# Kernel optimization log

Measured on AMD Instinct MI355X. Metric: run time of the kernel, lower is better.

The kernel has to match this reference:

```python
import jax, jax.numpy as jnp
import numpy as np

N = 100000      # nodes
E = 1600000     # edges (avg degree 16)
F_IN = 64
HID = 128
OUT = 64


def setup_inputs() -> dict:
    key = jax.random.key(0)
    ks = jax.random.split(key, 12)
    s = lambda k, i, o: jax.random.normal(k, (i, o), jnp.float32) / np.sqrt(i)
    x = jax.random.normal(ks[0], (N, F_IN), jnp.float32)
    edge_index = jax.random.randint(ks[1], (2, E), 0, N, dtype=jnp.int64)
    return {
        "x": x,
        "edge_index": edge_index,
        # conv1: SAGEConv(F_IN -> HID): lin_l (neighbors, with bias), lin_r (root)
        "W1n": s(ks[2], F_IN, HID), "b1n": jnp.zeros((HID,), jnp.float32),
        "W1r": s(ks[3], F_IN, HID),
        # lin1: Linear(F_IN -> HID)
        "Wl1": s(ks[4], F_IN, HID), "bl1": jnp.zeros((HID,), jnp.float32),
        # conv2: SAGEConv(HID -> OUT)
        "W2n": s(ks[5], HID, OUT), "b2n": jnp.zeros((OUT,), jnp.float32),
        "W2r": s(ks[6], HID, OUT),
        # lin2: Linear(HID -> OUT)
        "Wl2": s(ks[7], HID, OUT), "bl2": jnp.zeros((OUT,), jnp.float32),
    }


def _sage(x, src, dst, Wn, bn, Wr):
    # mean aggregation of source-node features at destination nodes
    msg = x[src]                                             # [E, F]
    agg = jax.ops.segment_sum(msg, dst, num_segments=N)      # [N, F]
    deg = jax.ops.segment_sum(jnp.ones((src.shape[0],), x.dtype), dst,
                              num_segments=N)                # [N]
    mean = agg / jnp.maximum(deg, 1.0)[:, None]
    return mean @ Wn + bn + x @ Wr


def reference(x, edge_index, W1n, b1n, W1r, Wl1, bl1, W2n, b2n, W2r, Wl2, bl2):
    src, dst = edge_index[0], edge_index[1]
    h = _sage(x, src, dst, W1n, b1n, W1r) + (x @ Wl1 + bl1)
    h = jax.nn.relu(h)
    out = _sage(h, src, dst, W2n, b2n, W2r) + (h @ Wl2 + bl2)
    return out
```

## Files before the change

### kernel.cpp

```cpp
#include <hip/hip_runtime.h>


#define NN 100000
#define NE 1600000
#define NSB 98
#define CAP2 18432
#define EPB 6250
#define MB 256
#define WPB 128

typedef __attribute__((ext_vector_type(8))) __bf16 bf16x8;
typedef __attribute__((ext_vector_type(4))) float f32x4;

__device__ __forceinline__ float b2f(unsigned short u) {
    unsigned v = ((unsigned)u) << 16;
    float f;
    __builtin_memcpy(&f, &v, 4);
    return f;
}
__device__ __forceinline__ float b2f_lo(unsigned v) {
    unsigned w = v << 16;
    float f;
    __builtin_memcpy(&f, &w, 4);
    return f;
}
__device__ __forceinline__ float b2f_hi(unsigned v) {
    unsigned w = v & 0xFFFF0000u;
    float f;
    __builtin_memcpy(&f, &w, 4);
    return f;
}
__device__ __forceinline__ unsigned short f2b(float f) {
    unsigned u;
    __builtin_memcpy(&u, &f, 4);
    u += 0x7FFFu + ((u >> 16) & 1u);
    return (unsigned short)(u >> 16);
}

__global__ void sniff_kernel(const int* __restrict__ ei,
                             const unsigned int* __restrict__ xw,
                             int* __restrict__ flags, int* __restrict__ cntP) {
    __shared__ int s_or[256];
    __shared__ int s_cnt[256];
    int tid = threadIdx.x;
    if (tid < NSB) cntP[tid * 16] = 0;
    s_or[tid] = ei[2 * tid + 1];
    unsigned e = (xw[tid] >> 7) & 0xFFu;
    s_cnt[tid] = (e > 0x85u) ? 1 : 0;
    __syncthreads();
    for (int s = 128; s > 0; s >>= 1) {
        if (tid < s) { s_or[tid] |= s_or[tid + s]; s_cnt[tid] += s_cnt[tid + s]; }
        __syncthreads();
    }
    if (tid == 0) {
        flags[0] = (s_or[0] == 0) ? 1 : 0;
        flags[1] = (s_cnt[0] >= 32) ? 1 : 0;
    }
}

__global__ __launch_bounds__(256) void prep_kernel(
    const void* __restrict__ x, const int* __restrict__ flags,
    const void* W1n, const void* W1r, const void* Wl1,
    const void* b1n, const void* bl1,
    const void* W2n, const void* W2r, const void* Wl2,
    const void* b2n, const void* bl2,
    unsigned short* __restrict__ Wt1g, unsigned short* __restrict__ Wt2g,
    float* __restrict__ bias1, float* __restrict__ bias2,
    unsigned int* __restrict__ xbu) {
    bool fp32 = flags[1] != 0;
    int tid = threadIdx.x;
    if (blockIdx.x >= WPB) {
        int t = (blockIdx.x - WPB) * 256 + tid;
        if (t >= NN * 8) return;
        if (fp32) {
            const float4* xf = (const float4*)x;
            float4 a = xf[2 * t], b = xf[2 * t + 1];
            uint4 o;
            o.x = f2b(a.x) | ((unsigned)f2b(a.y) << 16);
            o.y = f2b(a.z) | ((unsigned)f2b(a.w) << 16);
            o.z = f2b(b.x) | ((unsigned)f2b(b.y) << 16);
            o.w = f2b(b.z) | ((unsigned)f2b(b.w) << 16);
            ((uint4*)xbu)[t] = o;
        } else {
            ((uint4*)xbu)[t] = ((const uint4*)x)[t];
        }
        return;
    }
    auto rd = [&](const void* p, int i) -> float {
        return fp32 ? ((const float*)p)[i] : b2f(((const unsigned short*)p)[i]);
    };
    if (blockIdx.x < 64) {
        int idx = blockIdx.x * 256 + tid;
        int c = idx >> 7, k = idx & 127;
        float v = (k < 64) ? rd(W1n, k * 128 + c)
                           : rd(W1r, (k - 64) * 128 + c) + rd(Wl1, (k - 64) * 128 + c);
        Wt1g[c * 128 + k] = f2b(v);
        if (blockIdx.x == 0 && tid < 128) bias1[tid] = rd(b1n, tid) + rd(bl1, tid);
    } else {
        int idx = (blockIdx.x - 64) * 256 + tid;
        int c = idx >> 7, k = idx & 127;
        float v = (c < 64) ? rd(W2n, k * 64 + c)
                           : rd(W2r, k * 64 + (c - 64)) + rd(Wl2, k * 64 + (c - 64));
        Wt2g[c * 128 + k] = f2b(v);
        if (blockIdx.x == 64 && tid < 64) bias2[tid] = rd(b2n, tid) + rd(bl2, tid);
    }
}


__global__ __launch_bounds__(512) void bscatter_kernel(
    const int* __restrict__ ei, const int* __restrict__ flags,
    int* __restrict__ cntP, int* __restrict__ ebuf) {
    __shared__ int lh[NSB];
    __shared__ int lbase[NSB];
    int t = threadIdx.x;
    if (t < NSB) lh[t] = 0;
    __syncthreads();
    int e0 = blockIdx.x * EPB;
    bool i64 = flags[0] != 0;
    for (int i = t; i < EPB; i += 512) {
        int e = e0 + i;
        int d = i64 ? (int)((const long long*)ei)[NE + e] : ei[NE + e];
        atomicAdd(&lh[d >> 10], 1);
    }
    __syncthreads();
    if (t < NSB) {
        int c = lh[t];
        lbase[t] = c ? atomicAdd(&cntP[t * 16], c) : 0;
        lh[t] = 0;
    }
    __syncthreads();
    for (int i = t; i < EPB; i += 512) {
        int e = e0 + i;
        int s, d;
        if (i64) { const long long* q = (const long long*)ei; s = (int)q[e]; d = (int)q[NE + e]; }
        else     { s = ei[e]; d = ei[NE + e]; }
        int sb = d >> 10;
        int r = lbase[sb] + atomicAdd(&lh[sb], 1);
        if (r < CAP2) ebuf[sb * CAP2 + r] = (s << 10) | (d & 1023);
    }
}

__global__ __launch_bounds__(512) void csr_build_kernel(
    const int* __restrict__ ebuf, const int* __restrict__ cntP,
    int* __restrict__ rpack, int* __restrict__ csr) {
    __shared__ int lcnt[1024];
    __shared__ int lsum[512];
    __shared__ int lcur[1024];
    int t = threadIdx.x, b = blockIdx.x;
    lcnt[t] = 0; lcnt[t + 512] = 0;
    __syncthreads();
    int base = b * CAP2;
    int cnt = min(cntP[b * 16], CAP2);
    for (int i = t; i < cnt; i += 512) atomicAdd(&lcnt[ebuf[base + i] & 1023], 1);
    __syncthreads();
    int c0 = lcnt[2 * t], c1 = lcnt[2 * t + 1];
    lsum[t] = c0 + c1;
    __syncthreads();
    for (int off = 1; off < 512; off <<= 1) {
        int v = lsum[t];
        int add = (t >= off) ? lsum[t - off] : 0;
        __syncthreads();
        lsum[t] = v + add;
        __syncthreads();
    }
    int excl = (t == 0) ? 0 : lsum[t - 1];
    int ex0 = excl, ex1 = excl + c0;
    lcur[2 * t] = ex0; lcur[2 * t + 1] = ex1;
    int d0 = b * 1024 + 2 * t;
    if (d0 < NN)     rpack[d0]     = ((base + ex0) << 8) | min(c0, 255);
    if (d0 + 1 < NN) rpack[d0 + 1] = ((base + ex1) << 8) | min(c1, 255);
    __syncthreads();
    for (int i = t; i < cnt; i += 512) {
        int pk = ebuf[base + i];
        int r = atomicAdd(&lcur[pk & 1023], 1);
        csr[base + r] = pk >> 10;
    }
}


__device__ __forceinline__ void gather_acc(
    const unsigned short* __restrict__ feat, const int* __restrict__ csr,
    int base, int deg, int fo, float* acc) {
    int t = 0;
    for (; t + 8 <= deg; t += 8) {
        int i0 = csr[base + t],     i1 = csr[base + t + 1];
        int i2 = csr[base + t + 2], i3 = csr[base + t + 3];
        int i4 = csr[base + t + 4], i5 = csr[base + t + 5];
        int i6 = csr[base + t + 6], i7 = csr[base + t + 7];
        bf16x8 v0 = *(const bf16x8*)(feat + (size_t)i0 * 64 + fo);
        bf16x8 v1 = *(const bf16x8*)(feat + (size_t)i1 * 64 + fo);
        bf16x8 v2 = *(const bf16x8*)(feat + (size_t)i2 * 64 + fo);
        bf16x8 v3 = *(const bf16x8*)(feat + (size_t)i3 * 64 + fo);
        bf16x8 v4 = *(const bf16x8*)(feat + (size_t)i4 * 64 + fo);
        bf16x8 v5 = *(const bf16x8*)(feat + (size_t)i5 * 64 + fo);
        bf16x8 v6 = *(const bf16x8*)(feat + (size_t)i6 * 64 + fo);
        bf16x8 v7 = *(const bf16x8*)(feat + (size_t)i7 * 64 + fo);
#pragma unroll
        for (int k = 0; k < 8; ++k)
            acc[k] += (((float)v0[k] + (float)v1[k]) + ((float)v2[k] + (float)v3[k]))
                    + (((float)v4[k] + (float)v5[k]) + ((float)v6[k] + (float)v7[k]));
    }
    for (; t + 4 <= deg; t += 4) {
        int i0 = csr[base + t],     i1 = csr[base + t + 1];
        int i2 = csr[base + t + 2], i3 = csr[base + t + 3];
        bf16x8 v0 = *(const bf16x8*)(feat + (size_t)i0 * 64 + fo);
        bf16x8 v1 = *(const bf16x8*)(feat + (size_t)i1 * 64 + fo);
        bf16x8 v2 = *(const bf16x8*)(feat + (size_t)i2 * 64 + fo);
        bf16x8 v3 = *(const bf16x8*)(feat + (size_t)i3 * 64 + fo);
#pragma unroll
        for (int k = 0; k < 8; ++k)
            acc[k] += ((float)v0[k] + (float)v1[k]) + ((float)v2[k] + (float)v3[k]);
    }
    for (; t < deg; ++t) {
        int i = csr[base + t];
        bf16x8 v = *(const bf16x8*)(feat + (size_t)i * 64 + fo);
#pragma unroll
        for (int k = 0; k < 8; ++k) acc[k] += (float)v[k];
    }
}

__global__ __launch_bounds__(256) void agg1_kernel(
    const unsigned short* __restrict__ feat, const int* __restrict__ rpack,
    const int* __restrict__ csr, unsigned int* __restrict__ mean1u) {
    int wid = threadIdx.x >> 6, lane = threadIdx.x & 63;
    int slot = lane >> 3, fo = (lane & 7) * 8;
    int d = (blockIdx.x * 4 + wid) * 8 + slot;
    int dd = min(d, NN - 1);
    int rp = rpack[dd];
    int base = rp >> 8;
    int deg = rp & 255;
    float acc[8];
#pragma unroll
    for (int k = 0; k < 8; ++k) acc[k] = 0.f;
    gather_acc(feat, csr, base, deg, fo, acc);
    if (d < NN) {
        float r = 1.0f / fmaxf((float)deg, 1.0f);
        uint4 o;
        o.x = f2b(acc[0] * r) | ((unsigned)f2b(acc[1] * r) << 16);
        o.y = f2b(acc[2] * r) | ((unsigned)f2b(acc[3] * r) << 16);
        o.z = f2b(acc[4] * r) | ((unsigned)f2b(acc[5] * r) << 16);
        o.w = f2b(acc[6] * r) | ((unsigned)f2b(acc[7] * r) << 16);
        *(uint4*)(mean1u + (size_t)d * 32 + (lane & 7) * 4) = o;
    }
}

__global__ __launch_bounds__(256) void agg2_kernel(
    const unsigned short* __restrict__ p, const int* __restrict__ rpack,
    const int* __restrict__ csr, const unsigned int* __restrict__ sfu,
    const float* __restrict__ bias2, const int* __restrict__ flags,
    void* __restrict__ out) {
    int wid = threadIdx.x >> 6, lane = threadIdx.x & 63;
    int slot = lane >> 3, fo = (lane & 7) * 8;
    int d = (blockIdx.x * 4 + wid) * 8 + slot;
    int dd = min(d, NN - 1);
    int rp = rpack[dd];
    int base = rp >> 8;
    int deg = rp & 255;
    float acc[8];
#pragma unroll
    for (int k = 0; k < 8; ++k) acc[k] = 0.f;
    gather_acc(p, csr, base, deg, fo, acc);
    if (d < NN) {
        float r = 1.0f / fmaxf((float)deg, 1.0f);
        uint4 sv = *(const uint4*)(sfu + (size_t)d * 32 + (lane & 7) * 4);
        float4 bA = *(const float4*)(bias2 + fo);
        float4 bB = *(const float4*)(bias2 + fo + 4);
        float v0 = acc[0] * r + b2f_lo(sv.x) + bA.x;
        float v1 = acc[1] * r + b2f_hi(sv.x) + bA.y;
        float v2 = acc[2] * r + b2f_lo(sv.y) + bA.z;
        float v3 = acc[3] * r + b2f_hi(sv.y) + bA.w;
        float v4 = acc[4] * r + b2f_lo(sv.z) + bB.x;
        float v5 = acc[5] * r + b2f_hi(sv.z) + bB.y;
        float v6 = acc[6] * r + b2f_lo(sv.w) + bB.z;
        float v7 = acc[7] * r + b2f_hi(sv.w) + bB.w;
        if (flags[1]) {
            float* op = (float*)out + (size_t)d * 64 + fo;
            *(float4*)op = make_float4(v0, v1, v2, v3);
            *(float4*)(op + 4) = make_float4(v4, v5, v6, v7);
        } else {
            uint4 o;
            o.x = f2b(v0) | ((unsigned)f2b(v1) << 16);
            o.y = f2b(v2) | ((unsigned)f2b(v3) << 16);
            o.z = f2b(v4) | ((unsigned)f2b(v5) << 16);
            o.w = f2b(v6) | ((unsigned)f2b(v7) << 16);
            *(uint4*)((unsigned int*)out + (size_t)d * 32 + (lane & 7) * 4) = o;
        }
    }
}

__global__ __launch_bounds__(512, 2) void gemmF_kernel(
    const unsigned short* __restrict__ mean1,
    const unsigned short* __restrict__ xb,
    const unsigned short* __restrict__ Wt1g, const float* __restrict__ bias1,
    const unsigned short* __restrict__ Wt2g,
    unsigned short* __restrict__ p, unsigned short* __restrict__ sf) {
    __shared__ unsigned short Wt1s[128 * 136];
    __shared__ unsigned short Wt2s[128 * 136];
    __shared__ unsigned short hs[MB * 136];
    int tid = threadIdx.x;
    int wid = tid >> 6, lane = tid & 63;
    int m = lane & 15, g = lane >> 4;
    int row0 = blockIdx.x * MB + wid * 32;

    bf16x8 a_frag[2][4];
#pragma unroll
    for (int t = 0; t < 2; ++t) {
        int arow = min(row0 + t * 16 + m, NN - 1);
#pragma unroll
        for (int kt = 0; kt < 4; ++kt) {
            int k0 = kt * 32 + g * 8;
            a_frag[t][kt] = (k0 < 64)
                ? *(const bf16x8*)(mean1 + (size_t)arow * 64 + k0)
                : *(const bf16x8*)(xb + (size_t)arow * 64 + (k0 - 64));
        }
    }

    for (int idx = tid; idx < 4096; idx += 512) {
        int c = (idx >> 4) & 127, ch = idx & 15;
        if (idx < 2048)
            *(bf16x8*)&Wt1s[c * 136 + ch * 8] = *(const bf16x8*)&Wt1g[c * 128 + ch * 8];
        else
            *(bf16x8*)&Wt2s[c * 136 + ch * 8] = *(const bf16x8*)&Wt2g[c * 128 + ch * 8];
    }
    __syncthreads();

    f32x4 acc[2][8];
#pragma unroll
    for (int t = 0; t < 2; ++t)
#pragma unroll
        for (int nt = 0; nt < 8; ++nt) acc[t][nt] = (f32x4){0.f, 0.f, 0.f, 0.f};

#pragma unroll
    for (int kt = 0; kt < 4; ++kt) {
        int k0 = kt * 32 + g * 8;
        bf16x8 b[8];
#pragma unroll
        for (int nt = 0; nt < 8; ++nt)
            b[nt] = *(const bf16x8*)(&Wt1s[(nt * 16 + m) * 136 + k0]);
#pragma unroll
        for (int nt = 0; nt < 8; ++nt) {
            acc[0][nt] = __builtin_amdgcn_mfma_f32_16x16x32_bf16(a_frag[0][kt], b[nt], acc[0][nt], 0, 0, 0);
            acc[1][nt] = __builtin_amdgcn_mfma_f32_16x16x32_bf16(a_frag[1][kt], b[nt], acc[1][nt], 0, 0, 0);
        }
    }

#pragma unroll
    for (int t = 0; t < 2; ++t)
#pragma unroll
        for (int nt = 0; nt < 8; ++nt) {
            int col = nt * 16 + m;
            float bias = bias1[col];
#pragma unroll
            for (int r = 0; r < 4; ++r) {
                float v = fmaxf(acc[t][nt][r] + bias, 0.0f);
                hs[(wid * 32 + t * 16 + g * 4 + r) * 136 + col] = f2b(v);
            }
        }

    bf16x8 a2[2][4];
#pragma unroll
    for (int t = 0; t < 2; ++t)
#pragma unroll
        for (int kt = 0; kt < 4; ++kt)
            a2[t][kt] = *(const bf16x8*)(&hs[(wid * 32 + t * 16 + m) * 136 + kt * 32 + g * 8]);

#pragma unroll
    for (int t = 0; t < 2; ++t)
#pragma unroll
        for (int nt = 0; nt < 8; ++nt) acc[t][nt] = (f32x4){0.f, 0.f, 0.f, 0.f};

#pragma unroll
    for (int kt = 0; kt < 4; ++kt) {
        int k0 = kt * 32 + g * 8;
        bf16x8 b[8];
#pragma unroll
        for (int nt = 0; nt < 8; ++nt)
            b[nt] = *(const bf16x8*)(&Wt2s[(nt * 16 + m) * 136 + k0]);
#pragma unroll
        for (int nt = 0; nt < 8; ++nt) {
            acc[0][nt] = __builtin_amdgcn_mfma_f32_16x16x32_bf16(a2[0][kt], b[nt], acc[0][nt], 0, 0, 0);
            acc[1][nt] = __builtin_amdgcn_mfma_f32_16x16x32_bf16(a2[1][kt], b[nt], acc[1][nt], 0, 0, 0);
        }
    }

#pragma unroll
    for (int t = 0; t < 2; ++t)
#pragma unroll
        for (int nt = 0; nt < 8; ++nt) {
            int col = nt * 16 + m;
#pragma unroll
            for (int r = 0; r < 4; ++r) {
                int row2 = row0 + t * 16 + g * 4 + r;
                if (row2 < NN) {
                    float v = acc[t][nt][r];
                    if (col < 64) p[(size_t)row2 * 64 + col] = f2b(v);
                    else          sf[(size_t)row2 * 64 + (col - 64)] = f2b(v);
                }
            }
        }
}

extern "C" void kernel_launch(void* const* d_in, const int* in_sizes, int n_in,
                              void* d_out, int out_size, void* d_ws, size_t ws_size,
                              hipStream_t stream) {
    const void* x   = d_in[0];
    const int*  ei  = (const int*)d_in[1];
    const void* W1n = d_in[2];
    const void* b1n = d_in[3];
    const void* W1r = d_in[4];
    const void* Wl1 = d_in[5];
    const void* bl1 = d_in[6];
    const void* W2n = d_in[7];
    const void* b2n = d_in[8];
    const void* W2r = d_in[9];
    const void* Wl2 = d_in[10];
    const void* bl2 = d_in[11];

    char* ws = (char*)d_ws;
    int*            flags = (int*)(ws + 0);
    int*            cntP  = (int*)(ws + 1024);
    int*            rpack = (int*)(ws + 8192);
    float*          bias1 = (float*)(ws + 409600);
    float*          bias2 = (float*)(ws + 410112);
    unsigned short* Wt1g  = (unsigned short*)(ws + 410368);
    unsigned short* Wt2g  = (unsigned short*)(ws + 443136);
    int*            csr   = (int*)(ws + 475904);
    unsigned short* xb    = (unsigned short*)(ws + 7701248);
    unsigned short* p     = xb;
    unsigned short* mean1 = (unsigned short*)(ws + 20501248);
    unsigned short* sf    = (unsigned short*)(ws + 33301248);
    int*            ebuf  = (int*)(ws + 46101248);

    (void)in_sizes; (void)n_in; (void)out_size; (void)ws_size;

    sniff_kernel<<<1, 256, 0, stream>>>(ei, (const unsigned int*)x, flags, cntP);
    prep_kernel<<<WPB + (NN * 8 + 255) / 256, 256, 0, stream>>>(
        x, flags, W1n, W1r, Wl1, b1n, bl1, W2n, W2r, Wl2, b2n, bl2,
        Wt1g, Wt2g, bias1, bias2, (unsigned int*)xb);
    bscatter_kernel<<<256, 512, 0, stream>>>(ei, flags, cntP, ebuf);
    csr_build_kernel<<<NSB, 512, 0, stream>>>(ebuf, cntP, rpack, csr);
    agg1_kernel<<<(NN + 31) / 32, 256, 0, stream>>>(xb, rpack, csr, (unsigned int*)mean1);
    gemmF_kernel<<<(NN + MB - 1) / MB, 512, 0, stream>>>(mean1, xb, Wt1g, bias1, Wt2g, p, sf);
    agg2_kernel<<<(NN + 31) / 32, 256, 0, stream>>>(p, rpack, csr, (const unsigned int*)sf,
                                                    bias2, flags, d_out);
}
```

Baseline: 232.2 us.

## Fuse sniff, prep and edge bucketing into one front kernel

Merges the dtype-sniff, weight/input conversion and edge bucket-scatter kernels into one launch with role-partitioned blocks. Each block recomputes the int64 or fp32 detection locally, and the counter reset moves to a memset. Scatter blocks cache destination indices in shared memory so the second pass does not re-read them from global memory. The extra LDS per block may lower occupancy for the scatter role, and every block repeats the small sniff reduction.

```diff
diff --git a/kernel.cpp b/kernel.cpp
--- a/kernel.cpp
+++ b/kernel.cpp
@@ -7,7 +7,10 @@
 #define CAP2 18432
 #define EPB 6250
 #define MB 256
-#define WPB 128
+#define BSB 256
+#define W1B 32
+#define W2B 32
+#define XBLK ((NN * 8 + 511) / 512)
 
 typedef __attribute__((ext_vector_type(8))) __bf16 bf16x8;
 typedef __attribute__((ext_vector_type(4))) float f32x4;
@@ -37,106 +40,106 @@
     return (unsigned short)(u >> 16);
 }
 
-__global__ void sniff_kernel(const int* __restrict__ ei,
-                             const unsigned int* __restrict__ xw,
-                             int* __restrict__ flags, int* __restrict__ cntP) {
-    __shared__ int s_or[256];
-    __shared__ int s_cnt[256];
-    int tid = threadIdx.x;
-    if (tid < NSB) cntP[tid * 16] = 0;
-    s_or[tid] = ei[2 * tid + 1];
-    unsigned e = (xw[tid] >> 7) & 0xFFu;
-    s_cnt[tid] = (e > 0x85u) ? 1 : 0;
-    __syncthreads();
-    for (int s = 128; s > 0; s >>= 1) {
-        if (tid < s) { s_or[tid] |= s_or[tid + s]; s_cnt[tid] += s_cnt[tid + s]; }
-        __syncthreads();
-    }
-    if (tid == 0) {
-        flags[0] = (s_or[0] == 0) ? 1 : 0;
-        flags[1] = (s_cnt[0] >= 32) ? 1 : 0;
-    }
-}
-
-__global__ __launch_bounds__(256) void prep_kernel(
-    const void* __restrict__ x, const int* __restrict__ flags,
+__global__ __launch_bounds__(512) void front_kernel(
+    const void* __restrict__ x, const int* __restrict__ ei,
     const void* W1n, const void* W1r, const void* Wl1,
     const void* b1n, const void* bl1,
     const void* W2n, const void* W2r, const void* Wl2,
     const void* b2n, const void* bl2,
     unsigned short* __restrict__ Wt1g, unsigned short* __restrict__ Wt2g,
     float* __restrict__ bias1, float* __restrict__ bias2,
-    unsigned int* __restrict__ xbu) {
-    bool fp32 = flags[1] != 0;
-    int tid = threadIdx.x;
-    if (blockIdx.x >= WPB) {
-        int t = (blockIdx.x - WPB) * 256 + tid;
-        if (t >= NN * 8) return;
-        if (fp32) {
-            const float4* xf = (const float4*)x;
-            float4 a = xf[2 * t], b = xf[2 * t + 1];
-            uint4 o;
-            o.x = f2b(a.x) | ((unsigned)f2b(a.y) << 16);
-            o.y = f2b(a.z) | ((unsigned)f2b(a.w) << 16);
-            o.z = f2b(b.x) | ((unsigned)f2b(b.y) << 16);
-            o.w = f2b(b.z) | ((unsigned)f2b(b.w) << 16);
-            ((uint4*)xbu)[t] = o;
-        } else {
-            ((uint4*)xbu)[t] = ((const uint4*)x)[t];
+    unsigned int* __restrict__ xbu,
+    int* __restrict__ flags, int* __restrict__ cntP, int* __restrict__ ebuf) {
+    __shared__ int lh[NSB];
+    __shared__ int lbase[NSB];
+    __shared__ int ldst[EPB];
+    __shared__ int sred[256];
+    int t = threadIdx.x;
+    int b = blockIdx.x;
+
+    if (b < BSB) {
+        if (t < 256) sred[t] = ei[2 * t + 1];
+        if (t < NSB) lh[t] = 0;
+        __syncthreads();
+        for (int s = 128; s > 0; s >>= 1) {
+            if (t < s) sred[t] |= sred[t + s];
+            __syncthreads();
+        }
+        bool i64 = (sred[0] == 0);
+        int e0 = b * EPB;
+        for (int i = t; i < EPB; i += 512) {
+            int e = e0 + i;
+            int d = i64 ? (int)((const long long*)ei)[NE + e] : ei[NE + e];
+            ldst[i] = d;
+            atomicAdd(&lh[d >> 10], 1);
+        }
+        __syncthreads();
+        if (t < NSB) {
+            int c = lh[t];
+            lbase[t] = c ? atomicAdd(&cntP[t * 16], c) : 0;
+            lh[t] = 0;
+        }
+        __syncthreads();
+        for (int i = t; i < EPB; i += 512) {
+            int e = e0 + i;
+            int s = i64 ? (int)((const long long*)ei)[e] : ei[e];
+            int d = ldst[i];
+            int sb = d >> 10;
+            int r = lbase[sb] + atomicAdd(&lh[sb], 1);
+            if (r < CAP2) ebuf[sb * CAP2 + r] = (s << 10) | (d & 1023);
         }
         return;
     }
+
+    const unsigned int* xw = (const unsigned int*)x;
+    if (t < 256) {
+        unsigned e = (xw[t] >> 7) & 0xFFu;
+        sred[t] = (e > 0x85u) ? 1 : 0;
+    }
+    __syncthreads();
+    for (int s = 128; s > 0; s >>= 1) {
+        if (t < s) sred[t] += sred[t + s];
+        __syncthreads();
+    }
+    bool fp32 = sred[0] >= 32;
     auto rd = [&](const void* p, int i) -> float {
         return fp32 ? ((const float*)p)[i] : b2f(((const unsigned short*)p)[i]);
     };
-    if (blockIdx.x < 64) {
-        int idx = blockIdx.x * 256 + tid;
+
+    if (b < BSB + W1B) {
+        int idx = (b - BSB) * 512 + t;
         int c = idx >> 7, k = idx & 127;
         float v = (k < 64) ? rd(W1n, k * 128 + c)
                            : rd(W1r, (k - 64) * 128 + c) + rd(Wl1, (k - 64) * 128 + c);
         Wt1g[c * 128 + k] = f2b(v);
-        if (blockIdx.x == 0 && tid < 128) bias1[tid] = rd(b1n, tid) + rd(bl1, tid);
-    } else {
-        int idx = (blockIdx.x - 64) * 256 + tid;
+        if (b == BSB) {
+            if (t < 128) bias1[t] = rd(b1n, t) + rd(bl1, t);
+            if (t == 0) flags[1] = fp32 ? 1 : 0;
+        }
+        return;
+    }
+    if (b < BSB + W1B + W2B) {
+        int idx = (b - BSB - W1B) * 512 + t;
         int c = idx >> 7, k = idx & 127;
         float v = (c < 64) ? rd(W2n, k * 64 + c)
                            : rd(W2r, k * 64 + (c - 64)) + rd(Wl2, k * 64 + (c - 64));
         Wt2g[c * 128 + k] = f2b(v);
-        if (blockIdx.x == 64 && tid < 64) bias2[tid] = rd(b2n, tid) + rd(bl2, tid);
-    }
-}
-
-
-__global__ __launch_bounds__(512) void bscatter_kernel(
-    const int* __restrict__ ei, const int* __restrict__ flags,
-    int* __restrict__ cntP, int* __restrict__ ebuf) {
-    __shared__ int lh[NSB];
-    __shared__ int lbase[NSB];
-    int t = threadIdx.x;
-    if (t < NSB) lh[t] = 0;
-    __syncthreads();
-    int e0 = blockIdx.x * EPB;
-    bool i64 = flags[0] != 0;
-    for (int i = t; i < EPB; i += 512) {
-        int e = e0 + i;
-        int d = i64 ? (int)((const long long*)ei)[NE + e] : ei[NE + e];
-        atomicAdd(&lh[d >> 10], 1);
-    }
-    __syncthreads();
-    if (t < NSB) {
-        int c = lh[t];
-        lbase[t] = c ? atomicAdd(&cntP[t * 16], c) : 0;
-        lh[t] = 0;
-    }
-    __syncthreads();
-    for (int i = t; i < EPB; i += 512) {
-        int e = e0 + i;
-        int s, d;
-        if (i64) { const long long* q = (const long long*)ei; s = (int)q[e]; d = (int)q[NE + e]; }
-        else     { s = ei[e]; d = ei[NE + e]; }
-        int sb = d >> 10;
-        int r = lbase[sb] + atomicAdd(&lh[sb], 1);
-        if (r < CAP2) ebuf[sb * CAP2 + r] = (s << 10) | (d & 1023);
+        if (b == BSB + W1B && t < 64) bias2[t] = rd(b2n, t) + rd(bl2, t);
+        return;
+    }
+    int tt = (b - BSB - W1B - W2B) * 512 + t;
+    if (tt >= NN * 8) return;
+    if (fp32) {
+        const float4* xf = (const float4*)x;
+        float4 a = xf[2 * tt], c = xf[2 * tt + 1];
+        uint4 o;
+        o.x = f2b(a.x) | ((unsigned)f2b(a.y) << 16);
+        o.y = f2b(a.z) | ((unsigned)f2b(a.w) << 16);
+        o.z = f2b(c.x) | ((unsigned)f2b(c.y) << 16);
+        o.w = f2b(c.z) | ((unsigned)f2b(c.w) << 16);
+        ((uint4*)xbu)[tt] = o;
+    } else {
+        ((uint4*)xbu)[tt] = ((const uint4*)x)[tt];
     }
 }
 
@@ -433,11 +436,10 @@
 
     (void)in_sizes; (void)n_in; (void)out_size; (void)ws_size;
 
-    sniff_kernel<<<1, 256, 0, stream>>>(ei, (const unsigned int*)x, flags, cntP);
-    prep_kernel<<<WPB + (NN * 8 + 255) / 256, 256, 0, stream>>>(
-        x, flags, W1n, W1r, Wl1, b1n, bl1, W2n, W2r, Wl2, b2n, bl2,
-        Wt1g, Wt2g, bias1, bias2, (unsigned int*)xb);
-    bscatter_kernel<<<256, 512, 0, stream>>>(ei, flags, cntP, ebuf);
+    hipMemsetAsync(cntP, 0, NSB * 16 * sizeof(int), stream);
+    front_kernel<<<BSB + W1B + W2B + XBLK, 512, 0, stream>>>(
+        x, ei, W1n, W1r, Wl1, b1n, bl1, W2n, W2r, Wl2, b2n, bl2,
+        Wt1g, Wt2g, bias1, bias2, (unsigned int*)xb, flags, cntP, ebuf);
     csr_build_kernel<<<NSB, 512, 0, stream>>>(ebuf, cntP, rpack, csr);
     agg1_kernel<<<(NN + 31) / 32, 256, 0, stream>>>(xb, rpack, csr, (unsigned int*)mean1);
     gemmF_kernel<<<(NN + MB - 1) / MB, 512, 0, stream>>>(mean1, xb, Wt1g, bias1, Wt2g, p, sf);
```

Result: faster. 223.1 us (-3.9%).
